# Kernel tuning notes

Hardware: AMD Instinct MI355X
Metric: run time of the kernel (lower is better)

The kernel has to match this reference:

```python
import jax, jax.numpy as jnp
import numpy as np

D_MODEL = 2048
N_HEADS = 16
HEAD_DIM = D_MODEL // N_HEADS
SCALE = HEAD_DIM ** -0.5
LN_EPS = 1e-5
N_LAYERS = 24


def _layernorm(x, g, b):
    mu = jnp.mean(x, axis=-1, keepdims=True)
    var = jnp.mean(jnp.square(x - mu), axis=-1, keepdims=True)
    return (x - mu) * jax.lax.rsqrt(var + LN_EPS) * g + b


def _split_heads(x):  # [B,S,D] -> [B,H,S,hd]
    B, S, _ = x.shape
    return x.reshape(B, S, N_HEADS, HEAD_DIM).transpose(0, 2, 1, 3)


def setup_inputs() -> dict:
    key = jax.random.key(0)
    ks = jax.random.split(key, 12)
    B, St, Si = 2, 2048, 1024
    std_qkv = D_MODEL ** -0.5
    std_o = (2 * N_LAYERS) ** -0.5
    return {
        "q_text": jax.random.normal(ks[0], (B, St, D_MODEL), jnp.float32),
        "q_image": jax.random.normal(ks[1], (B, Si, D_MODEL), jnp.float32),
        "k_text": jax.random.normal(ks[2], (B, St, D_MODEL), jnp.float32),
        "k_image": jax.random.normal(ks[3], (B, Si, D_MODEL), jnp.float32),
        "Wq": jax.random.normal(ks[4], (D_MODEL, D_MODEL), jnp.float32) * std_qkv,
        "Wk": jax.random.normal(ks[5], (D_MODEL, D_MODEL), jnp.float32) * std_qkv,
        "Wv": jax.random.normal(ks[6], (D_MODEL, D_MODEL), jnp.float32) * std_qkv,
        "Wo": jax.random.normal(ks[7], (D_MODEL, D_MODEL), jnp.float32) * std_o,
        "ln_text_g": jnp.ones((D_MODEL,), jnp.float32),
        "ln_text_b": jnp.zeros((D_MODEL,), jnp.float32),
        "ln_image_g": jnp.ones((D_MODEL,), jnp.float32),
        "ln_image_b": jnp.zeros((D_MODEL,), jnp.float32),
    }


def reference(q_text, q_image, k_text, k_image, Wq, Wk, Wv, Wo,
              ln_text_g, ln_text_b, ln_image_g, ln_image_b):
    # Normalize each key modality once, project to K/V, concat along seq.
    kt = _layernorm(k_text, ln_text_g, ln_text_b)
    ki = _layernorm(k_image, ln_image_g, ln_image_b)
    concat_k = jnp.concatenate([_split_heads(kt @ Wk.T), _split_heads(ki @ Wk.T)], axis=2)
    concat_v = jnp.concatenate([_split_heads(kt @ Wv.T), _split_heads(ki @ Wv.T)], axis=2)

    def attend(q, g, b):
        B, S, _ = q.shape
        qn = _layernorm(q, g, b)
        qh = _split_heads(qn @ Wq.T) * SCALE            # [B,H,Sq,hd]
        scores = jnp.einsum('bhqd,bhkd->bhqk', qh, concat_k)
        attn = jax.nn.softmax(scores.astype(jnp.float32), axis=-1).astype(q.dtype)
        out = jnp.einsum('bhqk,bhkd->bhqd', attn, concat_v)
        out = out.transpose(0, 2, 1, 3).reshape(B, S, D_MODEL)
        return out @ Wo.T

    out_text = attend(q_text, ln_text_g, ln_text_b)
    out_image = attend(q_image, ln_image_g, ln_image_b)
    return (out_text, out_image)
```

## Files before the change

kernel.cpp:

```cpp
#include <hip/hip_runtime.h>

typedef __attribute__((ext_vector_type(8))) short bf16x8;
typedef __attribute__((ext_vector_type(4))) float f32x4;
typedef __attribute__((ext_vector_type(8))) unsigned short u16x8;

#define D_MODEL 2048
#define NH 16
#define HD 128
#define SKV 3072
#define QK_SCALE 0.08838834764831845f
#define LOG2E 1.4426950408889634f
#define DEFER_THR 11.5413f

__device__ __forceinline__ unsigned short f2bf(float f) {
  unsigned int u = __float_as_uint(f);
  u += 0x7fffu + ((u >> 16) & 1u);
  return (unsigned short)(u >> 16);
}
__device__ __forceinline__ float exp2hw(float x) {
  float r; asm("v_exp_f32 %0, %1" : "=v"(r) : "v"(x)); return r;
}
__device__ __forceinline__ unsigned int cvtpk(float lo, float hi) {
  unsigned int r; asm("v_cvt_pk_bf16_f32 %0, %1, %2" : "=v"(r) : "v"(lo), "v"(hi)); return r;
}

typedef __attribute__((address_space(1))) void as1_void;
typedef __attribute__((address_space(3))) void as3_void;
__device__ __forceinline__ void gload_lds16(const void* g, void* l) {
  __builtin_amdgcn_global_load_lds((as1_void*)g, (as3_void*)l, 16, 0, 0);
}

#define MFMA16(a, b, c) __builtin_amdgcn_mfma_f32_16x16x32_bf16((a), (b), (c), 0, 0, 0)

__global__ __launch_bounds__(256) void cvt_w_kernel(
    const float* __restrict__ s0, const float* __restrict__ s1,
    const float* __restrict__ s2, const float* __restrict__ s3,
    unsigned short* __restrict__ dstbase) {
  const int y = blockIdx.y;
  const float* src = (y == 0) ? s0 : (y == 1) ? s1 : (y == 2) ? s2 : s3;
  const float scale = (y == 0) ? (QK_SCALE * LOG2E) : 1.0f;
  unsigned short* dst = dstbase + (size_t)y * 4194304;
  int i = blockIdx.x * 256 + threadIdx.x;
  const float4* s = (const float4*)src + (size_t)i * 2;
  float4 a = s[0], b = s[1];
  u16x8 r;
  r[0] = f2bf(a.x * scale); r[1] = f2bf(a.y * scale);
  r[2] = f2bf(a.z * scale); r[3] = f2bf(a.w * scale);
  r[4] = f2bf(b.x * scale); r[5] = f2bf(b.y * scale);
  r[6] = f2bf(b.z * scale); r[7] = f2bf(b.w * scale);
  *((u16x8*)dst + i) = r;
}

__global__ __launch_bounds__(256) void ln_kernel(
    const float* __restrict__ x, const float* __restrict__ gw,
    const float* __restrict__ bw, unsigned short* __restrict__ out,
    int spb, int orpb, int obase) {
  const int row = blockIdx.x;
  const int t = threadIdx.x;
  const int b = row / spb, s = row - b * spb;
  const float* xr = x + (size_t)row * D_MODEL;
  unsigned short* orow = out + ((size_t)b * orpb + obase + s) * D_MODEL;

  float4 v0 = *(const float4*)(xr + t * 8);
  float4 v1 = *(const float4*)(xr + t * 8 + 4);
  float sum = v0.x + v0.y + v0.z + v0.w + v1.x + v1.y + v1.z + v1.w;
  float sq  = v0.x*v0.x + v0.y*v0.y + v0.z*v0.z + v0.w*v0.w
            + v1.x*v1.x + v1.y*v1.y + v1.z*v1.z + v1.w*v1.w;
#pragma unroll
  for (int o = 32; o > 0; o >>= 1) {
    sum += __shfl_down(sum, o);
    sq  += __shfl_down(sq, o);
  }
  __shared__ float red[8];
  const int wv = t >> 6, l = t & 63;
  if (l == 0) { red[wv] = sum; red[4 + wv] = sq; }
  __syncthreads();
  sum = red[0] + red[1] + red[2] + red[3];
  sq  = red[4] + red[5] + red[6] + red[7];
  const float mu = sum * (1.0f / 2048.0f);
  const float var = sq * (1.0f / 2048.0f) - mu * mu;
  const float rs = rsqrtf(var + 1e-5f);

  float4 g0 = *(const float4*)(gw + t * 8);
  float4 g1 = *(const float4*)(gw + t * 8 + 4);
  float4 b0 = *(const float4*)(bw + t * 8);
  float4 b1 = *(const float4*)(bw + t * 8 + 4);
  u16x8 r;
  r[0] = f2bf((v0.x - mu) * rs * g0.x + b0.x);
  r[1] = f2bf((v0.y - mu) * rs * g0.y + b0.y);
  r[2] = f2bf((v0.z - mu) * rs * g0.z + b0.z);
  r[3] = f2bf((v0.w - mu) * rs * g0.w + b0.w);
  r[4] = f2bf((v1.x - mu) * rs * g1.x + b1.x);
  r[5] = f2bf((v1.y - mu) * rs * g1.y + b1.y);
  r[6] = f2bf((v1.z - mu) * rs * g1.z + b1.z);
  r[7] = f2bf((v1.w - mu) * rs * g1.w + b1.w);
  *(u16x8*)(orow + t * 8) = r;
}

__global__ __launch_bounds__(256, 3) void gemm128_kernel(
    const unsigned short* __restrict__ Aq, const unsigned short* __restrict__ Akv,
    const unsigned short* __restrict__ Wq, const unsigned short* __restrict__ Wk,
    const unsigned short* __restrict__ Wv,
    void* __restrict__ d0, void* __restrict__ d1,
    void* __restrict__ d2, void* __restrict__ d3, int mode) {
  __shared__ unsigned short lds[3][2][4096];

  const int tid = threadIdx.x;
  const int wid = tid >> 6, l = tid & 63;
  const int wm = wid >> 1, wn = wid & 1;
  const int fr = l & 15, fg = l >> 4;

  const int cpx = gridDim.x >> 3;
  int wg = (blockIdx.x & 7) * cpx + (blockIdx.x >> 3);

  const unsigned short* A = Aq;
  const unsigned short* W = Wq;
  int emode = mode;
  if (mode == 10) {
    int mat = wg / 768; wg -= mat * 768;
    if (mat == 0)      { emode = 0; }
    else if (mat == 1) { emode = 3; A = Akv; W = Wk; }
    else               { emode = 1; A = Akv; W = Wv; }
  }
  const int bm = wg >> 4, bn = wg & 15;

  const unsigned short* ga = A + (size_t)(bm * 128 + wid * 32 + (l >> 2)) * 2048 + (l & 3) * 8;
  const unsigned short* gb = W + (size_t)(bn * 128 + wid * 32 + (l >> 2)) * 2048 + (l & 3) * 8;

#define STAGE(buf, kt) do {                                   \
    const int _ko = (kt) * 32;                                \
    unsigned short* _la = &lds[(buf)][0][wid * 1024];         \
    unsigned short* _lb = &lds[(buf)][1][wid * 1024];         \
    gload_lds16(ga + _ko,             _la);                   \
    gload_lds16(ga + _ko + 16 * 2048, _la + 512);             \
    gload_lds16(gb + _ko,             _lb);                   \
    gload_lds16(gb + _ko + 16 * 2048, _lb + 512);             \
  } while (0)

  f32x4 acc[4][4] = {};

  STAGE(0, 0);
  STAGE(1, 1);
  asm volatile("s_waitcnt vmcnt(4)" ::: "memory");
  __builtin_amdgcn_s_barrier();

  int cur = 0;
  for (int kt = 0; kt < 64; ++kt) {
    bf16x8 af[4], bfr[4];
#pragma unroll
    for (int mi = 0; mi < 4; ++mi)
      af[mi] = *(const bf16x8*)&lds[cur][0][(wm * 64 + mi * 16 + fr) * 32 + fg * 8];
#pragma unroll
    for (int ni = 0; ni < 4; ++ni)
      bfr[ni] = *(const bf16x8*)&lds[cur][1][(wn * 64 + ni * 16 + fr) * 32 + fg * 8];

    if (kt < 62) {
      int sb = cur + 2; if (sb >= 3) sb -= 3;
      STAGE(sb, kt + 2);
    }

    __builtin_amdgcn_s_setprio(1);
#pragma unroll
    for (int mi = 0; mi < 4; ++mi)
#pragma unroll
      for (int ni = 0; ni < 4; ++ni)
        acc[mi][ni] = MFMA16(af[mi], bfr[ni], acc[mi][ni]);
    __builtin_amdgcn_s_setprio(0);

    __builtin_amdgcn_sched_barrier(0);
    if (kt < 62) {
      asm volatile("s_waitcnt vmcnt(4)" ::: "memory");
      __builtin_amdgcn_s_barrier();
    } else if (kt < 63) {
      asm volatile("s_waitcnt vmcnt(0)" ::: "memory");
      __builtin_amdgcn_s_barrier();
    }
    ++cur; if (cur >= 3) cur = 0;
  }
#undef STAGE

#pragma unroll
  for (int mi = 0; mi < 4; ++mi) {
#pragma unroll
    for (int r = 0; r < 4; ++r) {
      int row = bm * 128 + wm * 64 + mi * 16 + fg * 4 + r;
#pragma unroll
      for (int ni = 0; ni < 4; ++ni) {
        int col = bn * 128 + wn * 64 + ni * 16 + fr;
        float v = acc[mi][ni][r];
        if (emode == 2) {
          ((float*)d0)[(size_t)row * 2048 + col] = v;
        } else if (emode == 0) {
          int hh = col >> 7, d = col & 127;
          if (row < 4096) {
            int b = row >> 11, s = row & 2047;
            ((unsigned short*)d0)[((size_t)(b * NH + hh) * 2048 + s) * 128 + d] = f2bf(v);
          } else {
            int rr = row - 4096, b = rr >> 10, s = rr & 1023;
            ((unsigned short*)d1)[((size_t)(b * NH + hh) * 1024 + s) * 128 + d] = f2bf(v);
          }
        } else {
          int b = row / 3072, s = row - b * 3072;
          int hh = col >> 7, d = col & 127;
          size_t bh = (size_t)(b * NH + hh);
          if (emode == 3) {
            ((unsigned short*)d2)[(bh * 3072 + s) * 128 + (d ^ ((s & 7) << 3))] = f2bf(v);
          } else {
            int ssw = (s & ~31) | ((s & 31) ^ ((d & 3) << 3));
            ((unsigned short*)d3)[(bh * 128 + d) * (size_t)3072 + ssw] = f2bf(v);
          }
        }
      }
    }
  }
}

__global__ __launch_bounds__(256, 3) void attn_kernel(
    const unsigned short* __restrict__ Qt, const unsigned short* __restrict__ Qi,
    const unsigned short* __restrict__ Kh, const unsigned short* __restrict__ Vt,
    unsigned short* __restrict__ AOt, unsigned short* __restrict__ AOi) {
  __shared__ unsigned short Sh[20480];

  const int lin = blockIdx.x;
  const int w768 = (lin & 7) * 96 + (lin >> 3);
  const int qt24 = w768 % 24;
  const int hb   = w768 / 24;
  const int h = hb & 15, b = hb >> 4;
  const bool is_text = qt24 < 16;
  const int qt = is_text ? qt24 : qt24 - 16;
  const int Sq = is_text ? 2048 : 1024;
  const unsigned short* Qh = is_text ? Qt : Qi;
  unsigned short* AO = is_text ? AOt : AOi;

  const int tid = threadIdx.x;
  const int w = tid >> 6, l = tid & 63;
  const int fr = l & 15, fg = l >> 4;
  const size_t bh = (size_t)(b * NH + h);
  unsigned short* Pw = Sh + 16384 + w * 1024;

  const unsigned short* Qbase = Qh + (bh * Sq + (size_t)qt * 128 + w * 32) * HD;
  bf16x8 qf[2][4];
#pragma unroll
  for (int h2 = 0; h2 < 2; ++h2)
#pragma unroll
    for (int c = 0; c < 4; ++c)
      qf[h2][c] = *(const bf16x8*)(Qbase + (h2 * 16 + fr) * HD + c * 32 + fg * 8);

  f32x4 o[2][8] = {};
  float m[2]    = {-1e30f, -1e30f};
  float lsum[2] = {0.f, 0.f};

  const unsigned short* Kb = Kh + bh * (size_t)SKV * HD;
  const unsigned short* Vb = Vt + bh * (size_t)HD * SKV;

  const int swk = (fr & 7) << 3;
  const int swv = (fr & 3) << 3;

#define STAGE_K(kt, half) do {                                                   \
    unsigned short* _d = Sh + (half) * 4096 + w * 1024;                          \
    const unsigned short* _s = Kb + (size_t)((kt) * 32 + w * 8 + (l >> 4)) * 128 \
                               + (l & 15) * 8;                                   \
    gload_lds16(_s, _d);                                                         \
    gload_lds16(_s + 4 * 128, _d + 512);                                         \
  } while (0)
#define STAGE_V(kt, half) do {                                                   \
    unsigned short* _d = Sh + 8192 + (half) * 4096 + w * 1024;                   \
    const unsigned short* _s = Vb + (size_t)(w * 32 + (l >> 2)) * SKV            \
                               + (kt) * 32 + (l & 3) * 8;                        \
    gload_lds16(_s, _d);                                                         \
    gload_lds16(_s + 16 * SKV, _d + 512);                                        \
  } while (0)

  STAGE_K(0, 0);
  for (int kt = 0; kt < 96; ++kt) {
    const int half = kt & 1;
    STAGE_V(kt, half);
    asm volatile("s_waitcnt vmcnt(2)" ::: "memory");
    __builtin_amdgcn_s_barrier();

    const unsigned short* Ksc = Sh + half * 4096;
    f32x4 sT[2][2] = {};
#pragma unroll
    for (int j = 0; j < 2; ++j) {
      const int krb = (j * 16 + fr) * 128;
#pragma unroll
      for (int c = 0; c < 4; ++c) {
        bf16x8 kf = *(const bf16x8*)&Ksc[krb + ((c * 32 + fg * 8) ^ swk)];
        sT[0][j] = MFMA16(kf, qf[0][c], sT[0][j]);
        sT[1][j] = MFMA16(kf, qf[1][c], sT[1][j]);
      }
    }
    if (kt < 95) STAGE_K(kt + 1, half ^ 1);

#pragma unroll
    for (int h2 = 0; h2 < 2; ++h2) {
      float tm = fmaxf(fmaxf(fmaxf(sT[h2][0][0], sT[h2][0][1]),
                             fmaxf(sT[h2][0][2], sT[h2][0][3])),
                       fmaxf(fmaxf(sT[h2][1][0], sT[h2][1][1]),
                             fmaxf(sT[h2][1][2], sT[h2][1][3])));
      tm = fmaxf(tm, __shfl_xor(tm, 16));
      tm = fmaxf(tm, __shfl_xor(tm, 32));
      if (__any(tm - m[h2] > DEFER_THR)) {
        float mn = fmaxf(m[h2], tm);
        float al = exp2hw(m[h2] - mn);
#pragma unroll
        for (int nt = 0; nt < 8; ++nt) {
          f32x4 t = o[h2][nt];
          t[0] *= al; t[1] *= al; t[2] *= al; t[3] *= al;
          o[h2][nt] = t;
        }
        lsum[h2] *= al;
        m[h2] = mn;
      }
      const float mm = m[h2];
      float p00 = exp2hw(sT[h2][0][0] - mm), p01 = exp2hw(sT[h2][0][1] - mm);
      float p02 = exp2hw(sT[h2][0][2] - mm), p03 = exp2hw(sT[h2][0][3] - mm);
      float p10 = exp2hw(sT[h2][1][0] - mm), p11 = exp2hw(sT[h2][1][1] - mm);
      float p12 = exp2hw(sT[h2][1][2] - mm), p13 = exp2hw(sT[h2][1][3] - mm);
      lsum[h2] += (p00 + p01 + p02 + p03) + (p10 + p11 + p12 + p13);
      unsigned short* prow = &Pw[(h2 * 16 + fr) * 32];
      uint2 w0; w0.x = cvtpk(p00, p01); w0.y = cvtpk(p02, p03);
      uint2 w1; w1.x = cvtpk(p10, p11); w1.y = cvtpk(p12, p13);
      *(uint2*)(prow + ((fg * 4) ^ swv))      = w0;
      *(uint2*)(prow + ((16 + fg * 4) ^ swv)) = w1;
    }

    if (kt < 95) asm volatile("s_waitcnt vmcnt(2)" ::: "memory");
    else         asm volatile("s_waitcnt vmcnt(0)" ::: "memory");
    __builtin_amdgcn_s_barrier();

    asm volatile("s_waitcnt lgkmcnt(0)" ::: "memory");
    __builtin_amdgcn_sched_barrier(0);

    const unsigned short* Vsc = Sh + 8192 + half * 4096;
    bf16x8 pb[2];
#pragma unroll
    for (int h2 = 0; h2 < 2; ++h2)
      pb[h2] = *(const bf16x8*)&Pw[(h2 * 16 + fr) * 32 + ((fg * 8) ^ swv)];
#pragma unroll
    for (int nt = 0; nt < 8; ++nt) {
      bf16x8 vf = *(const bf16x8*)&Vsc[(nt * 16 + fr) * 32 + ((fg * 8) ^ swv)];
      o[0][nt] = MFMA16(vf, pb[0], o[0][nt]);
      o[1][nt] = MFMA16(vf, pb[1], o[1][nt]);
    }
    __builtin_amdgcn_s_barrier();
  }
#undef STAGE_K
#undef STAGE_V

  float inv[2];
#pragma unroll
  for (int h2 = 0; h2 < 2; ++h2) {
    float t = lsum[h2];
    t += __shfl_xor(t, 16);
    t += __shfl_xor(t, 32);
    inv[h2] = 1.0f / t;
  }
  unsigned short* Os = &Sh[w * 4096];
#pragma unroll
  for (int h2 = 0; h2 < 2; ++h2) {
    unsigned short* orow = &Os[(h2 * 16 + fr) * 128];
    const int sw8 = (fr & 7) << 3;
#pragma unroll
    for (int nt = 0; nt < 8; ++nt) {
      uint2 pk;
      pk.x = cvtpk(o[h2][nt][0] * inv[h2], o[h2][nt][1] * inv[h2]);
      pk.y = cvtpk(o[h2][nt][2] * inv[h2], o[h2][nt][3] * inv[h2]);
      *(uint2*)(orow + ((nt * 16 + fg * 4) ^ sw8)) = pk;
    }
  }
  asm volatile("s_waitcnt lgkmcnt(0)" ::: "memory");
  __builtin_amdgcn_sched_barrier(0);
  const int qr4 = l >> 4;
  const int dc = (l & 15) * 8;
  unsigned short* AObase = AO + ((size_t)b * Sq + (size_t)qt * 128 + w * 32) * D_MODEL + h * HD;
#pragma unroll
  for (int g = 0; g < 8; ++g) {
    const int row = g * 4 + qr4;
    bf16x8 v = *reinterpret_cast<const bf16x8*>(&Os[row * 128 + (dc ^ ((row & 7) << 3))]);
    *reinterpret_cast<bf16x8*>(&AObase[(size_t)row * D_MODEL + dc]) = v;
  }
}

extern "C" void kernel_launch(void* const* d_in, const int* in_sizes, int n_in,
                              void* d_out, int out_size, void* d_ws, size_t ws_size,
                              hipStream_t stream) {
  const float* q_text  = (const float*)d_in[0];
  const float* q_image = (const float*)d_in[1];
  const float* k_text  = (const float*)d_in[2];
  const float* k_image = (const float*)d_in[3];
  const float* Wq = (const float*)d_in[4];
  const float* Wk = (const float*)d_in[5];
  const float* Wv = (const float*)d_in[6];
  const float* Wo = (const float*)d_in[7];
  const float* ln_tg = (const float*)d_in[8];
  const float* ln_tb = (const float*)d_in[9];
  const float* ln_ig = (const float*)d_in[10];
  const float* ln_ib = (const float*)d_in[11];

  unsigned short* wq  = (unsigned short*)d_ws;
  unsigned short* wk  = wq  + 4194304;
  unsigned short* wv  = wk  + 4194304;
  unsigned short* wo  = wv  + 4194304;
  unsigned short* xqt = wo  + 4194304;
  unsigned short* xqi = xqt + 8388608;
  unsigned short* xk  = xqi + 4194304;
  unsigned short* qht = xk  + 12582912;
  unsigned short* qhi = qht + 8388608;
  unsigned short* kh  = qhi + 4194304;
  unsigned short* vt  = kh  + 12582912;
  const size_t needed = (size_t)(vt + 12582912 - wq) * 2;
  if (ws_size < needed) return;

  cvt_w_kernel<<<dim3(2048, 4), 256, 0, stream>>>(Wq, Wk, Wv, Wo, wq);

  ln_kernel<<<4096, 256, 0, stream>>>(q_text,  ln_tg, ln_tb, xqt, 2048, 2048, 0);
  ln_kernel<<<2048, 256, 0, stream>>>(q_image, ln_ig, ln_ib, xqi, 1024, 1024, 0);
  ln_kernel<<<4096, 256, 0, stream>>>(k_text,  ln_tg, ln_tb, xk, 2048, 3072, 0);
  ln_kernel<<<2048, 256, 0, stream>>>(k_image, ln_ig, ln_ib, xk, 1024, 3072, 2048);

  gemm128_kernel<<<2304, 256, 0, stream>>>(xqt, xk, wq, wk, wv, qht, qhi, kh, vt, 10);

  attn_kernel<<<768, 256, 0, stream>>>(qht, qhi, kh, vt, xqt, xqi);

  gemm128_kernel<<<768, 256, 0, stream>>>(xqt, nullptr, wo, nullptr, nullptr,
                                          d_out, nullptr, nullptr, nullptr, 2);
}
```

Measured before the change: 531.8 us.

## Replace 128x128 GEMM with 256x256 tile, 8-wave, XOR-swizzled LDS pipeline

Replaces the 128x128 tile GEMM (4 waves, triple-buffered BK=32) with a 256x256 tile kernel using 8 waves, double-buffered BK=64 and an XOR-swizzled LDS layout. Loads are staged in interleaved halves between MFMA phases, and the V-transpose epilogue now writes packed bf16 quads. The goal is higher arithmetic intensity per LDS byte, fewer bank conflicts and cheaper stores. The cost is far fewer workgroups (576 and 192 on 256 CUs), which risks wave-quantization tail effects and higher register pressure.

Result: faster. 499.3 us (-6.1%).

```diff
diff --git a/kernel.cpp b/kernel.cpp
--- a/kernel.cpp
+++ b/kernel.cpp
@@ -97,117 +97,180 @@
   *(u16x8*)(orow + t * 8) = r;
 }
 
-__global__ __launch_bounds__(256, 3) void gemm128_kernel(
+__global__ __launch_bounds__(512, 2) void gemm256p_kernel(
     const unsigned short* __restrict__ Aq, const unsigned short* __restrict__ Akv,
     const unsigned short* __restrict__ Wq, const unsigned short* __restrict__ Wk,
     const unsigned short* __restrict__ Wv,
     void* __restrict__ d0, void* __restrict__ d1,
     void* __restrict__ d2, void* __restrict__ d3, int mode) {
-  __shared__ unsigned short lds[3][2][4096];
+  __shared__ unsigned short lds2[2][32768];
 
   const int tid = threadIdx.x;
   const int wid = tid >> 6, l = tid & 63;
-  const int wm = wid >> 1, wn = wid & 1;
+  const int wm = wid >> 2, wn = wid & 3;
   const int fr = l & 15, fg = l >> 4;
+  const int swz = (fr & 7) << 3;
 
   const int cpx = gridDim.x >> 3;
-  int wg = (blockIdx.x & 7) * cpx + (blockIdx.x >> 3);
+  int wg = ((int)blockIdx.x & 7) * cpx + ((int)blockIdx.x >> 3);
 
   const unsigned short* A = Aq;
   const unsigned short* W = Wq;
   int emode = mode;
   if (mode == 10) {
-    int mat = wg / 768; wg -= mat * 768;
+    int mat = wg / 192; wg -= mat * 192;
     if (mat == 0)      { emode = 0; }
     else if (mat == 1) { emode = 3; A = Akv; W = Wk; }
     else               { emode = 1; A = Akv; W = Wv; }
   }
-  const int bm = wg >> 4, bn = wg & 15;
-
-  const unsigned short* ga = A + (size_t)(bm * 128 + wid * 32 + (l >> 2)) * 2048 + (l & 3) * 8;
-  const unsigned short* gb = W + (size_t)(bn * 128 + wid * 32 + (l >> 2)) * 2048 + (l & 3) * 8;
-
-#define STAGE(buf, kt) do {                                   \
-    const int _ko = (kt) * 32;                                \
-    unsigned short* _la = &lds[(buf)][0][wid * 1024];         \
-    unsigned short* _lb = &lds[(buf)][1][wid * 1024];         \
-    gload_lds16(ga + _ko,             _la);                   \
-    gload_lds16(ga + _ko + 16 * 2048, _la + 512);             \
-    gload_lds16(gb + _ko,             _lb);                   \
-    gload_lds16(gb + _ko + 16 * 2048, _lb + 512);             \
+  const int bm = wg >> 3, bn = wg & 7;
+
+  const int lr = l >> 3;
+  const int kc = (l & 7) ^ lr;
+  const unsigned short* gaBase = A + (size_t)(bm * 256 + wid * 16 + lr) * 2048 + kc * 8;
+  const unsigned short* gbBase = W + (size_t)(bn * 256 + wid * 16 + lr) * 2048 + kc * 8;
+
+#define STAGEA(Lp, kt) do {                                        \
+    unsigned short* _d = (Lp) + wid * 1024;                        \
+    const unsigned short* _s = gaBase + (size_t)(kt) * 64;         \
+    gload_lds16(_s,               _d);                             \
+    gload_lds16(_s + 8 * 2048,    _d + 512);                       \
+    gload_lds16(_s + 128 * 2048,  _d + 8192);                      \
+    gload_lds16(_s + 136 * 2048,  _d + 8704);                      \
   } while (0)
-
-  f32x4 acc[4][4] = {};
-
-  STAGE(0, 0);
-  STAGE(1, 1);
-  asm volatile("s_waitcnt vmcnt(4)" ::: "memory");
+#define STAGEB(Lp, kt) do {                                        \
+    unsigned short* _d = (Lp) + 16384 + wid * 1024;                \
+    const unsigned short* _s = gbBase + (size_t)(kt) * 64;         \
+    gload_lds16(_s,               _d);                             \
+    gload_lds16(_s + 8 * 2048,    _d + 512);                       \
+    gload_lds16(_s + 128 * 2048,  _d + 8192);                      \
+    gload_lds16(_s + 136 * 2048,  _d + 8704);                      \
+  } while (0)
+
+  f32x4 acc[8][4] = {};
+  bf16x8 af[8][2], bf01[2][2], bf23[2][2];
+
+  STAGEA(&lds2[0][0], 0); STAGEB(&lds2[0][0], 0);
+  STAGEA(&lds2[1][0], 1); STAGEB(&lds2[1][0], 1);
+  asm volatile("s_waitcnt vmcnt(8)" ::: "memory");
   __builtin_amdgcn_s_barrier();
 
-  int cur = 0;
-  for (int kt = 0; kt < 64; ++kt) {
-    bf16x8 af[4], bfr[4];
+  for (int t = 0; t < 32; ++t) {
+    unsigned short* Lp = &lds2[t & 1][0];
+    const unsigned short* Ab = Lp + wm * 8192;
+    const unsigned short* Bb = Lp + 16384 + (wn >> 1) * 8192 + (wn & 1) * 4096;
+
 #pragma unroll
     for (int mi = 0; mi < 4; ++mi)
-      af[mi] = *(const bf16x8*)&lds[cur][0][(wm * 64 + mi * 16 + fr) * 32 + fg * 8];
-#pragma unroll
-    for (int ni = 0; ni < 4; ++ni)
-      bfr[ni] = *(const bf16x8*)&lds[cur][1][(wn * 64 + ni * 16 + fr) * 32 + fg * 8];
-
-    if (kt < 62) {
-      int sb = cur + 2; if (sb >= 3) sb -= 3;
-      STAGE(sb, kt + 2);
-    }
-
+#pragma unroll
+      for (int ks = 0; ks < 2; ++ks)
+        af[mi][ks] = *(const bf16x8*)&Ab[(mi * 16 + fr) * 64 + ((ks * 32 + fg * 8) ^ swz)];
+#pragma unroll
+    for (int ni = 0; ni < 2; ++ni)
+#pragma unroll
+      for (int ks = 0; ks < 2; ++ks)
+        bf01[ni][ks] = *(const bf16x8*)&Bb[(ni * 16 + fr) * 64 + ((ks * 32 + fg * 8) ^ swz)];
     __builtin_amdgcn_s_setprio(1);
 #pragma unroll
     for (int mi = 0; mi < 4; ++mi)
 #pragma unroll
-      for (int ni = 0; ni < 4; ++ni)
-        acc[mi][ni] = MFMA16(af[mi], bfr[ni], acc[mi][ni]);
+      for (int ni = 0; ni < 2; ++ni)
+#pragma unroll
+        for (int ks = 0; ks < 2; ++ks)
+          acc[mi][ni] = MFMA16(af[mi][ks], bf01[ni][ks], acc[mi][ni]);
     __builtin_amdgcn_s_setprio(0);
 
+#pragma unroll
+    for (int mi = 4; mi < 8; ++mi)
+#pragma unroll
+      for (int ks = 0; ks < 2; ++ks)
+        af[mi][ks] = *(const bf16x8*)&Ab[(mi * 16 + fr) * 64 + ((ks * 32 + fg * 8) ^ swz)];
+    __builtin_amdgcn_s_setprio(1);
+#pragma unroll
+    for (int mi = 4; mi < 8; ++mi)
+#pragma unroll
+      for (int ni = 0; ni < 2; ++ni)
+#pragma unroll
+        for (int ks = 0; ks < 2; ++ks)
+          acc[mi][ni] = MFMA16(af[mi][ks], bf01[ni][ks], acc[mi][ni]);
+    __builtin_amdgcn_s_setprio(0);
+    __builtin_amdgcn_s_barrier();
+
+#pragma unroll
+    for (int ni = 0; ni < 2; ++ni)
+#pragma unroll
+      for (int ks = 0; ks < 2; ++ks)
+        bf23[ni][ks] = *(const bf16x8*)&Bb[((ni + 2) * 16 + fr) * 64 + ((ks * 32 + fg * 8) ^ swz)];
+    if (t < 30) STAGEA(Lp, t + 2);
+    __builtin_amdgcn_s_setprio(1);
+#pragma unroll
+    for (int mi = 0; mi < 4; ++mi)
+#pragma unroll
+      for (int ni = 0; ni < 2; ++ni)
+#pragma unroll
+        for (int ks = 0; ks < 2; ++ks)
+          acc[mi][ni + 2] = MFMA16(af[mi][ks], bf23[ni][ks], acc[mi][ni + 2]);
+    __builtin_amdgcn_s_setprio(0);
+    __builtin_amdgcn_s_barrier();
+
+    if (t < 30) STAGEB(Lp, t + 2);
+    __builtin_amdgcn_s_setprio(1);
+#pragma unroll
+    for (int mi = 4; mi < 8; ++mi)
+#pragma unroll
+      for (int ni = 0; ni < 2; ++ni)
+#pragma unroll
+        for (int ks = 0; ks < 2; ++ks)
+          acc[mi][ni + 2] = MFMA16(af[mi][ks], bf23[ni][ks], acc[mi][ni + 2]);
+    __builtin_amdgcn_s_setprio(0);
     __builtin_amdgcn_sched_barrier(0);
-    if (kt < 62) {
-      asm volatile("s_waitcnt vmcnt(4)" ::: "memory");
-      __builtin_amdgcn_s_barrier();
-    } else if (kt < 63) {
-      asm volatile("s_waitcnt vmcnt(0)" ::: "memory");
-      __builtin_amdgcn_s_barrier();
-    }
-    ++cur; if (cur >= 3) cur = 0;
-  }
-#undef STAGE
-
-#pragma unroll
-  for (int mi = 0; mi < 4; ++mi) {
-#pragma unroll
-    for (int r = 0; r < 4; ++r) {
-      int row = bm * 128 + wm * 64 + mi * 16 + fg * 4 + r;
+    if (t < 30)       asm volatile("s_waitcnt vmcnt(8)" ::: "memory");
+    else if (t == 30) asm volatile("s_waitcnt vmcnt(0)" ::: "memory");
+    if (t < 31) __builtin_amdgcn_s_barrier();
+  }
+#undef STAGEA
+#undef STAGEB
+
+#pragma unroll
+  for (int mi = 0; mi < 8; ++mi) {
+    const int row0 = bm * 256 + wm * 128 + mi * 16 + fg * 4;
+    if (emode == 1) {
+      int b = row0 / 3072, s0 = row0 - b * 3072;
 #pragma unroll
       for (int ni = 0; ni < 4; ++ni) {
-        int col = bn * 128 + wn * 64 + ni * 16 + fr;
-        float v = acc[mi][ni][r];
-        if (emode == 2) {
-          ((float*)d0)[(size_t)row * 2048 + col] = v;
-        } else if (emode == 0) {
-          int hh = col >> 7, d = col & 127;
-          if (row < 4096) {
-            int b = row >> 11, s = row & 2047;
-            ((unsigned short*)d0)[((size_t)(b * NH + hh) * 2048 + s) * 128 + d] = f2bf(v);
+        int col = bn * 256 + wn * 64 + ni * 16 + fr;
+        int hh = col >> 7, d = col & 127;
+        size_t bh = (size_t)(b * NH + hh);
+        size_t idx = (bh * 128 + d) * (size_t)3072 + ((s0 & ~31) | ((s0 & 31) ^ ((d & 3) << 3)));
+        uint2 pk;
+        pk.x = cvtpk(acc[mi][ni][0], acc[mi][ni][1]);
+        pk.y = cvtpk(acc[mi][ni][2], acc[mi][ni][3]);
+        *(uint2*)((unsigned short*)d3 + idx) = pk;
+      }
+    } else {
+#pragma unroll
+      for (int r = 0; r < 4; ++r) {
+        int row = row0 + r;
+#pragma unroll
+        for (int ni = 0; ni < 4; ++ni) {
+          int col = bn * 256 + wn * 64 + ni * 16 + fr;
+          float v = acc[mi][ni][r];
+          if (emode == 2) {
+            ((float*)d0)[(size_t)row * 2048 + col] = v;
+          } else if (emode == 0) {
+            int hh = col >> 7, d = col & 127;
+            if (row < 4096) {
+              int b = row >> 11, s = row & 2047;
+              ((unsigned short*)d0)[((size_t)(b * NH + hh) * 2048 + s) * 128 + d] = f2bf(v);
+            } else {
+              int rr = row - 4096, b = rr >> 10, s = rr & 1023;
+              ((unsigned short*)d1)[((size_t)(b * NH + hh) * 1024 + s) * 128 + d] = f2bf(v);
+            }
           } else {
-            int rr = row - 4096, b = rr >> 10, s = rr & 1023;
-            ((unsigned short*)d1)[((size_t)(b * NH + hh) * 1024 + s) * 128 + d] = f2bf(v);
-          }
-        } else {
-          int b = row / 3072, s = row - b * 3072;
-          int hh = col >> 7, d = col & 127;
-          size_t bh = (size_t)(b * NH + hh);
-          if (emode == 3) {
+            int b = row / 3072, s = row - b * 3072;
+            int hh = col >> 7, d = col & 127;
+            size_t bh = (size_t)(b * NH + hh);
             ((unsigned short*)d2)[(bh * 3072 + s) * 128 + (d ^ ((s & 7) << 3))] = f2bf(v);
-          } else {
-            int ssw = (s & ~31) | ((s & 31) ^ ((d & 3) << 3));
-            ((unsigned short*)d3)[(bh * 128 + d) * (size_t)3072 + ssw] = f2bf(v);
           }
         }
       }
@@ -419,10 +482,10 @@
   ln_kernel<<<4096, 256, 0, stream>>>(k_text,  ln_tg, ln_tb, xk, 2048, 3072, 0);
   ln_kernel<<<2048, 256, 0, stream>>>(k_image, ln_ig, ln_ib, xk, 1024, 3072, 2048);
 
-  gemm128_kernel<<<2304, 256, 0, stream>>>(xqt, xk, wq, wk, wv, qht, qhi, kh, vt, 10);
+  gemm256p_kernel<<<576, 512, 0, stream>>>(xqt, xk, wq, wk, wv, qht, qhi, kh, vt, 10);
 
   attn_kernel<<<768, 256, 0, stream>>>(qht, qhi, kh, vt, xqt, xqi);
 
-  gemm128_kernel<<<768, 256, 0, stream>>>(xqt, nullptr, wo, nullptr, nullptr,
-                                          d_out, nullptr, nullptr, nullptr, 2);
-}
+  gemm256p_kernel<<<192, 512, 0, stream>>>(xqt, nullptr, wo, nullptr, nullptr,
+                                           d_out, nullptr, nullptr, nullptr, 2);
+}
```

## Enlarge GEMM tiles to 256x256 with 8 waves, LDS swizzle and register prefetch

Applied to the files above, without the earlier changes.

Replaces the 128x128, 4-wave GEMM with a 256x256-tile, 8-wave (512-thread) kernel. Each wave now computes a 128x64 sub-tile, which raises arithmetic intensity per staged byte. Loads are XOR-swizzled in LDS to avoid bank conflicts, and the next k-step's A/B fragments are prefetched into registers across the barrier. The V-transpose epilogue also packs four bf16 values per store. The cost is more registers and LDS per block and fewer blocks per grid (576 and 192), which may hurt occupancy and leave tail imbalance on the smaller output-projection GEMM.

After: 515.1 us. -3.1%, faster.

```diff
diff --git a/kernel.cpp b/kernel.cpp
--- a/kernel.cpp
+++ b/kernel.cpp
@@ -97,117 +97,152 @@
   *(u16x8*)(orow + t * 8) = r;
 }
 
-__global__ __launch_bounds__(256, 3) void gemm128_kernel(
+__global__ __launch_bounds__(512, 2) void gemm256r_kernel(
     const unsigned short* __restrict__ Aq, const unsigned short* __restrict__ Akv,
     const unsigned short* __restrict__ Wq, const unsigned short* __restrict__ Wk,
     const unsigned short* __restrict__ Wv,
     void* __restrict__ d0, void* __restrict__ d1,
     void* __restrict__ d2, void* __restrict__ d3, int mode) {
-  __shared__ unsigned short lds[3][2][4096];
+  __shared__ unsigned short lds3[3][16384];
 
   const int tid = threadIdx.x;
   const int wid = tid >> 6, l = tid & 63;
-  const int wm = wid >> 1, wn = wid & 1;
+  const int wm = wid >> 2, wn = wid & 3;
   const int fr = l & 15, fg = l >> 4;
+  const int rc = (fg * 8) ^ ((fr & 3) << 3);
 
   const int cpx = gridDim.x >> 3;
-  int wg = (blockIdx.x & 7) * cpx + (blockIdx.x >> 3);
+  int wg = ((int)blockIdx.x & 7) * cpx + ((int)blockIdx.x >> 3);
 
   const unsigned short* A = Aq;
   const unsigned short* W = Wq;
   int emode = mode;
   if (mode == 10) {
-    int mat = wg / 768; wg -= mat * 768;
+    int mat = wg / 192; wg -= mat * 192;
     if (mat == 0)      { emode = 0; }
     else if (mat == 1) { emode = 3; A = Akv; W = Wk; }
     else               { emode = 1; A = Akv; W = Wv; }
   }
-  const int bm = wg >> 4, bn = wg & 15;
-
-  const unsigned short* ga = A + (size_t)(bm * 128 + wid * 32 + (l >> 2)) * 2048 + (l & 3) * 8;
-  const unsigned short* gb = W + (size_t)(bn * 128 + wid * 32 + (l >> 2)) * 2048 + (l & 3) * 8;
-
-#define STAGE(buf, kt) do {                                   \
-    const int _ko = (kt) * 32;                                \
-    unsigned short* _la = &lds[(buf)][0][wid * 1024];         \
-    unsigned short* _lb = &lds[(buf)][1][wid * 1024];         \
-    gload_lds16(ga + _ko,             _la);                   \
-    gload_lds16(ga + _ko + 16 * 2048, _la + 512);             \
-    gload_lds16(gb + _ko,             _lb);                   \
-    gload_lds16(gb + _ko + 16 * 2048, _lb + 512);             \
+  const int bm = wg >> 3, bn = wg & 7;
+
+  const int lr = l >> 2;
+  const int gsw = ((l & 3) ^ (lr & 3)) * 8;
+  const unsigned short* gaBase = A + (size_t)(bm * 256 + wid * 32 + lr) * 2048 + gsw;
+  const unsigned short* gbBase = W + (size_t)(bn * 256 + wid * 32 + lr) * 2048 + gsw;
+
+#define STAGE(buf, kt) do {                                          \
+    unsigned short* _da = &lds3[(buf)][wid * 1024];                  \
+    unsigned short* _db = &lds3[(buf)][8192 + wid * 1024];           \
+    const unsigned short* _sa = gaBase + (size_t)(kt) * 32;          \
+    const unsigned short* _sb = gbBase + (size_t)(kt) * 32;          \
+    gload_lds16(_sa,             _da);                               \
+    gload_lds16(_sa + 16 * 2048, _da + 512);                         \
+    gload_lds16(_sb,             _db);                               \
+    gload_lds16(_sb + 16 * 2048, _db + 512);                         \
   } while (0)
 
-  f32x4 acc[4][4] = {};
+  f32x4 acc[8][4] = {};
+  bf16x8 af[8], bf01[2], bf23[2];
 
   STAGE(0, 0);
   STAGE(1, 1);
   asm volatile("s_waitcnt vmcnt(4)" ::: "memory");
   __builtin_amdgcn_s_barrier();
+#pragma unroll
+  for (int mi = 0; mi < 8; ++mi)
+    af[mi] = *(const bf16x8*)&lds3[0][(wm * 128 + mi * 16 + fr) * 32 + rc];
+#pragma unroll
+  for (int ni = 0; ni < 2; ++ni)
+    bf01[ni] = *(const bf16x8*)&lds3[0][8192 + (wn * 64 + ni * 16 + fr) * 32 + rc];
 
   int cur = 0;
-  for (int kt = 0; kt < 64; ++kt) {
-    bf16x8 af[4], bfr[4];
-#pragma unroll
-    for (int mi = 0; mi < 4; ++mi)
-      af[mi] = *(const bf16x8*)&lds[cur][0][(wm * 64 + mi * 16 + fr) * 32 + fg * 8];
-#pragma unroll
-    for (int ni = 0; ni < 4; ++ni)
-      bfr[ni] = *(const bf16x8*)&lds[cur][1][(wn * 64 + ni * 16 + fr) * 32 + fg * 8];
-
-    if (kt < 62) {
-      int sb = cur + 2; if (sb >= 3) sb -= 3;
-      STAGE(sb, kt + 2);
+  for (int t = 0; t < 64; ++t) {
+#pragma unroll
+    for (int ni = 0; ni < 2; ++ni)
+      bf23[ni] = *(const bf16x8*)&lds3[cur][8192 + (wn * 64 + (ni + 2) * 16 + fr) * 32 + rc];
+    if (t < 62) {
+      int stg = cur + 2; if (stg >= 3) stg -= 3;
+      STAGE(stg, t + 2);
     }
 
     __builtin_amdgcn_s_setprio(1);
 #pragma unroll
-    for (int mi = 0; mi < 4; ++mi)
-#pragma unroll
-      for (int ni = 0; ni < 4; ++ni)
-        acc[mi][ni] = MFMA16(af[mi], bfr[ni], acc[mi][ni]);
+    for (int mi = 0; mi < 8; ++mi)
+#pragma unroll
+      for (int ni = 0; ni < 2; ++ni)
+        acc[mi][ni] = MFMA16(af[mi], bf01[ni], acc[mi][ni]);
     __builtin_amdgcn_s_setprio(0);
 
+    __builtin_amdgcn_s_setprio(1);
+#pragma unroll
+    for (int mi = 0; mi < 8; ++mi)
+#pragma unroll
+      for (int ni = 0; ni < 2; ++ni)
+        acc[mi][ni + 2] = MFMA16(af[mi], bf23[ni], acc[mi][ni + 2]);
+    __builtin_amdgcn_s_setprio(0);
+
     __builtin_amdgcn_sched_barrier(0);
-    if (kt < 62) {
+    if (t < 62) {
       asm volatile("s_waitcnt vmcnt(4)" ::: "memory");
       __builtin_amdgcn_s_barrier();
-    } else if (kt < 63) {
+    } else if (t == 62) {
       asm volatile("s_waitcnt vmcnt(0)" ::: "memory");
       __builtin_amdgcn_s_barrier();
     }
-    ++cur; if (cur >= 3) cur = 0;
+
+    int nxt = cur + 1; if (nxt >= 3) nxt -= 3;
+    if (t < 63) {
+#pragma unroll
+      for (int mi = 0; mi < 8; ++mi)
+        af[mi] = *(const bf16x8*)&lds3[nxt][(wm * 128 + mi * 16 + fr) * 32 + rc];
+#pragma unroll
+      for (int ni = 0; ni < 2; ++ni)
+        bf01[ni] = *(const bf16x8*)&lds3[nxt][8192 + (wn * 64 + ni * 16 + fr) * 32 + rc];
+    }
+    cur = nxt;
   }
 #undef STAGE
 
 #pragma unroll
-  for (int mi = 0; mi < 4; ++mi) {
-#pragma unroll
-    for (int r = 0; r < 4; ++r) {
-      int row = bm * 128 + wm * 64 + mi * 16 + fg * 4 + r;
+  for (int mi = 0; mi < 8; ++mi) {
+    const int row0 = bm * 256 + wm * 128 + mi * 16 + fg * 4;
+    if (emode == 1) {
+      int b = row0 / 3072, s0 = row0 - b * 3072;
 #pragma unroll
       for (int ni = 0; ni < 4; ++ni) {
-        int col = bn * 128 + wn * 64 + ni * 16 + fr;
-        float v = acc[mi][ni][r];
-        if (emode == 2) {
-          ((float*)d0)[(size_t)row * 2048 + col] = v;
-        } else if (emode == 0) {
-          int hh = col >> 7, d = col & 127;
-          if (row < 4096) {
-            int b = row >> 11, s = row & 2047;
-            ((unsigned short*)d0)[((size_t)(b * NH + hh) * 2048 + s) * 128 + d] = f2bf(v);
+        int col = bn * 256 + wn * 64 + ni * 16 + fr;
+        int hh = col >> 7, d = col & 127;
+        size_t bh = (size_t)(b * NH + hh);
+        size_t idx = (bh * 128 + d) * (size_t)3072 + ((s0 & ~31) | ((s0 & 31) ^ ((d & 3) << 3)));
+        uint2 pk;
+        pk.x = cvtpk(acc[mi][ni][0], acc[mi][ni][1]);
+        pk.y = cvtpk(acc[mi][ni][2], acc[mi][ni][3]);
+        *(uint2*)((unsigned short*)d3 + idx) = pk;
+      }
+    } else {
+#pragma unroll
+      for (int r = 0; r < 4; ++r) {
+        int row = row0 + r;
+#pragma unroll
+        for (int ni = 0; ni < 4; ++ni) {
+          int col = bn * 256 + wn * 64 + ni * 16 + fr;
+          float v = acc[mi][ni][r];
+          if (emode == 2) {
+            ((float*)d0)[(size_t)row * 2048 + col] = v;
+          } else if (emode == 0) {
+            int hh = col >> 7, d = col & 127;
+            if (row < 4096) {
+              int b = row >> 11, s = row & 2047;
+              ((unsigned short*)d0)[((size_t)(b * NH + hh) * 2048 + s) * 128 + d] = f2bf(v);
+            } else {
+              int rr = row - 4096, b = rr >> 10, s = rr & 1023;
+              ((unsigned short*)d1)[((size_t)(b * NH + hh) * 1024 + s) * 128 + d] = f2bf(v);
+            }
           } else {
-            int rr = row - 4096, b = rr >> 10, s = rr & 1023;
-            ((unsigned short*)d1)[((size_t)(b * NH + hh) * 1024 + s) * 128 + d] = f2bf(v);
-          }
-        } else {
-          int b = row / 3072, s = row - b * 3072;
-          int hh = col >> 7, d = col & 127;
-          size_t bh = (size_t)(b * NH + hh);
-          if (emode == 3) {
+            int b = row / 3072, s = row - b * 3072;
+            int hh = col >> 7, d = col & 127;
+            size_t bh = (size_t)(b * NH + hh);
             ((unsigned short*)d2)[(bh * 3072 + s) * 128 + (d ^ ((s & 7) << 3))] = f2bf(v);
-          } else {
-            int ssw = (s & ~31) | ((s & 31) ^ ((d & 3) << 3));
-            ((unsigned short*)d3)[(bh * 128 + d) * (size_t)3072 + ssw] = f2bf(v);
           }
         }
       }
@@ -419,10 +454,10 @@
   ln_kernel<<<4096, 256, 0, stream>>>(k_text,  ln_tg, ln_tb, xk, 2048, 3072, 0);
   ln_kernel<<<2048, 256, 0, stream>>>(k_image, ln_ig, ln_ib, xk, 1024, 3072, 2048);
 
-  gemm128_kernel<<<2304, 256, 0, stream>>>(xqt, xk, wq, wk, wv, qht, qhi, kh, vt, 10);
+  gemm256r_kernel<<<576, 512, 0, stream>>>(xqt, xk, wq, wk, wv, qht, qhi, kh, vt, 10);
 
   attn_kernel<<<768, 256, 0, stream>>>(qht, qhi, kh, vt, xqt, xqi);
 
-  gemm128_kernel<<<768, 256, 0, stream>>>(xqt, nullptr, wo, nullptr, nullptr,
-                                          d_out, nullptr, nullptr, nullptr, 2);
-}
+  gemm256r_kernel<<<192, 512, 0, stream>>>(xqt, nullptr, wo, nullptr, nullptr,
+                                           d_out, nullptr, nullptr, nullptr, 2);
+}
```
